# Kernel tuning notes

Measured on AMD Instinct MI355X. Metric: run time of the kernel, lower is better.

## Reference

```python
import jax, jax.numpy as jnp
import numpy as np


def setup_inputs() -> dict:
    key = jax.random.key(0)
    kx, kw = jax.random.split(key)
    B, IN, OUT = 8192, 256, 16384
    x = jax.random.normal(kx, (B, IN), dtype=jnp.float32)
    weight = jax.random.normal(kw, (OUT, IN), dtype=jnp.float32)
    return {"x": x, "weight": weight}


def reference(x, weight):
    # Pairwise Euclidean distance ||x_b - w_o||_2 via expansion:
    temperature = 2.0
    x2 = jnp.sum(x * x, axis=1, keepdims=True)          # [B, 1]
    w2 = jnp.sum(weight * weight, axis=1)[None, :]       # [1, OUT]
    xw = x @ weight.T                                    # [B, OUT]
    d2 = jnp.maximum(x2 + w2 - 2.0 * xw, 0.0)            # clamp fp error
    dist = jnp.sqrt(d2)                                  # [B, OUT]
    return jax.nn.softmax(-temperature * dist, axis=1)
```

## Files before the change

kernel.cpp:

```cpp
#include <hip/hip_runtime.h>
#include <math.h>
#include <stdint.h>

#define M_ROWS 8192
#define N_COLS 16384
#define K_DIM  256
#define NTILE  (N_COLS / 128)
#define CHUNK  2048
#define NCHUNK 4

typedef _Float16 half8  __attribute__((ext_vector_type(8)));
typedef _Float16 half4v __attribute__((ext_vector_type(4)));
typedef float    vf4    __attribute__((ext_vector_type(4)));

__device__ __forceinline__ void gload16(const void* g, void* lds) {
  __builtin_amdgcn_global_load_lds(
      (__attribute__((address_space(1))) void*)(void*)g,
      (__attribute__((address_space(3))) void*)lds, 16, 0, 0);
}

__global__ __launch_bounds__(256) void prep_kernel(
    const float* __restrict__ x, const float* __restrict__ w,
    float* __restrict__ x2, float* __restrict__ w2,
    _Float16* __restrict__ xh, _Float16* __restrict__ wh) {
  int row  = blockIdx.x * 4 + (threadIdx.x >> 6);
  int lane = threadIdx.x & 63;
  const float* src; _Float16* dst; float* nrm;
  if (row < M_ROWS) {
    src = x + (size_t)row * K_DIM; dst = xh + (size_t)row * K_DIM; nrm = x2 + row;
  } else {
    int r = row - M_ROWS;
    src = w + (size_t)r * K_DIM; dst = wh + (size_t)r * K_DIM; nrm = w2 + r;
  }
  float4 v = ((const float4*)src)[lane];
  float s = v.x*v.x + v.y*v.y + v.z*v.z + v.w*v.w;
  #pragma unroll
  for (int off = 32; off > 0; off >>= 1) s += __shfl_down(s, off);
  if (lane == 0) *nrm = s;
  half4v h; h[0]=(_Float16)v.x; h[1]=(_Float16)v.y; h[2]=(_Float16)v.z; h[3]=(_Float16)v.w;
  ((half4v*)dst)[lane] = h;
}

template <int MODE>
__global__ __launch_bounds__(256, 2) void gemm_pass(
    const _Float16* __restrict__ A, const _Float16* __restrict__ Bm,
    const float* __restrict__ x2g, const float* __restrict__ w2g,
    const float* __restrict__ invg,
    float* __restrict__ partials,
    float* __restrict__ out) {
  __shared__ _Float16 As[128 * 64];
  __shared__ _Float16 Bs[128 * 64];
  __shared__ float x2s[128];
  __shared__ float w2s[128];
  __shared__ float invs[128];
  __shared__ float rowpart[2][128];

  int id   = blockIdx.x;
  int xcd  = id & 7;
  int rest = id >> 3;
  int ct   = xcd * 16 + (rest & 15);
  int rt   = rest >> 4;
  int brow = rt * 128;
  int bcol = ct * 128;

  int tid = threadIdx.x, lane = tid & 63, wid = tid >> 6;
  int wr = wid >> 1, wc = wid & 1;

  if (tid < 128) {
    x2s[tid] = x2g[brow + tid];
    if (MODE == 1) invs[tid] = invg[brow + tid];
  } else {
    w2s[tid - 128] = w2g[bcol + tid - 128];
  }

  vf4 acc[4][4] = {};

  for (int kk = 0; kk < K_DIM; kk += 64) {
    #pragma unroll
    for (int i = 0; i < 4; ++i) {
      int seg = wid * 4 + i;
      int r   = seg * 8 + (lane >> 3);
      gload16(A  + (size_t)(brow + r) * K_DIM + kk + (lane & 7) * 8, (char*)As + seg * 1024);
      gload16(Bm + (size_t)(bcol + r) * K_DIM + kk + (lane & 7) * 8, (char*)Bs + seg * 1024);
    }
    __syncthreads();

    #pragma unroll
    for (int ks = 0; ks < 2; ++ks) {
      half8 af[4], bf[4];
      #pragma unroll
      for (int m = 0; m < 4; ++m)
        af[m] = *(const half8*)&As[(wr*64 + m*16 + (lane & 15)) * 64 + ks*32 + (lane >> 4) * 8];
      #pragma unroll
      for (int n = 0; n < 4; ++n)
        bf[n] = *(const half8*)&Bs[(wc*64 + n*16 + (lane & 15)) * 64 + ks*32 + (lane >> 4) * 8];
      #pragma unroll
      for (int m = 0; m < 4; ++m)
        #pragma unroll
        for (int n = 0; n < 4; ++n)
          acc[m][n] = __builtin_amdgcn_mfma_f32_16x16x32_f16(af[m], bf[n], acc[m][n], 0, 0, 0);
    }
    __syncthreads();
  }

  if (MODE == 0) {
    #pragma unroll
    for (int m = 0; m < 4; ++m) {
      #pragma unroll
      for (int j = 0; j < 4; ++j) {
        int rl = wr * 64 + m * 16 + ((lane >> 4) << 2) + j;
        float x2v = x2s[rl];
        float sm = 0.f;
        #pragma unroll
        for (int n = 0; n < 4; ++n) {
          int cl = wc * 64 + n * 16 + (lane & 15);
          float d2 = fmaxf(x2v + w2s[cl] - 2.0f * acc[m][n][j], 0.0f);
          sm += __expf(-2.0f * sqrtf(d2));
        }
        sm += __shfl_xor(sm, 1);
        sm += __shfl_xor(sm, 2);
        sm += __shfl_xor(sm, 4);
        sm += __shfl_xor(sm, 8);
        if ((lane & 15) == 0) rowpart[wc][rl] = sm;
      }
    }
    __syncthreads();
    if (tid < 128)
      partials[(size_t)(brow + tid) * NTILE + ct] = rowpart[0][tid] + rowpart[1][tid];
  } else {
    #pragma unroll
    for (int m = 0; m < 4; ++m) {
      #pragma unroll
      for (int j = 0; j < 4; ++j) {
        int rl = wr * 64 + m * 16 + ((lane >> 4) << 2) + j;
        float x2v = x2s[rl];
        float inv = invs[rl];
        size_t rowbase = (size_t)(brow + rl) * N_COLS + bcol;
        #pragma unroll
        for (int n = 0; n < 4; ++n) {
          int cl = wc * 64 + n * 16 + (lane & 15);
          float d2 = fmaxf(x2v + w2s[cl] - 2.0f * acc[m][n][j], 0.0f);
          out[rowbase + cl] = __expf(-2.0f * sqrtf(d2)) * inv;
        }
      }
    }
  }
}

__global__ __launch_bounds__(256) void reduce_inv(
    const float* __restrict__ partials, float* __restrict__ invg) {
  int row  = blockIdx.x * 4 + (threadIdx.x >> 6);
  int lane = threadIdx.x & 63;
  const float* p = partials + (size_t)row * NTILE;
  float s = p[lane] + p[lane + 64];
  #pragma unroll
  for (int off = 32; off > 0; off >>= 1) s += __shfl_down(s, off);
  if (lane == 0) invg[row] = 1.0f / s;
}

template <bool WS>
__global__ __launch_bounds__(256, 2) void gemm_logit(
    const void* __restrict__ Aptr, const void* __restrict__ Bptr,
    const float* __restrict__ x2g, const float* __restrict__ w2g,
    float* __restrict__ out, int mbase) {
  __shared__ _Float16 As[128 * 64];
  __shared__ _Float16 Bs[128 * 64];
  __shared__ float x2s[128];
  __shared__ float w2s[128];

  int id  = blockIdx.x;
  int xcd = id & 7;
  int rt  = (id >> 3) & 15;
  int c2  = id >> 7;
  int brow = mbase + rt * 128;
  int bcol = (xcd * 16 + c2) * 128;

  int tid = threadIdx.x, lane = tid & 63, wid = tid >> 6;
  int wr = wid >> 1, wc = wid & 1;

  vf4 acc[4][4] = {};

  const float* xf = (const float*)Aptr;
  const float* wf = (const float*)Bptr;
  {
    const float* src = (tid < 128) ? xf + (size_t)(brow + tid) * K_DIM
                                   : wf + (size_t)(bcol + tid - 128) * K_DIM;
    float s = 0.f;
    for (int i = 0; i < 64; ++i) {
      float4 v = ((const float4*)src)[i];
      s += v.x*v.x + v.y*v.y + v.z*v.z + v.w*v.w;
    }
    if (tid < 128) x2s[tid] = s; else w2s[tid - 128] = s;
  }

  for (int kk = 0; kk < K_DIM; kk += 64) {
    #pragma unroll
    for (int i = 0; i < 8; ++i) {
      int idx = i * 256 + tid;
      int r = idx >> 4, kq = idx & 15;
      float4 va = ((const float4*)(xf + (size_t)(brow + r) * K_DIM + kk))[kq];
      float4 vb = ((const float4*)(wf + (size_t)(bcol + r) * K_DIM + kk))[kq];
      half4v ha; ha[0]=(_Float16)va.x; ha[1]=(_Float16)va.y; ha[2]=(_Float16)va.z; ha[3]=(_Float16)va.w;
      half4v hb; hb[0]=(_Float16)vb.x; hb[1]=(_Float16)vb.y; hb[2]=(_Float16)vb.z; hb[3]=(_Float16)vb.w;
      *(half4v*)&As[r * 64 + kq * 4] = ha;
      *(half4v*)&Bs[r * 64 + kq * 4] = hb;
    }
    __syncthreads();
    #pragma unroll
    for (int ks = 0; ks < 2; ++ks) {
      half8 af[4], bf[4];
      #pragma unroll
      for (int m = 0; m < 4; ++m)
        af[m] = *(const half8*)&As[(wr*64 + m*16 + (lane & 15)) * 64 + ks*32 + (lane >> 4) * 8];
      #pragma unroll
      for (int n = 0; n < 4; ++n)
        bf[n] = *(const half8*)&Bs[(wc*64 + n*16 + (lane & 15)) * 64 + ks*32 + (lane >> 4) * 8];
      #pragma unroll
      for (int m = 0; m < 4; ++m)
        #pragma unroll
        for (int n = 0; n < 4; ++n)
          acc[m][n] = __builtin_amdgcn_mfma_f32_16x16x32_f16(af[m], bf[n], acc[m][n], 0, 0, 0);
    }
    __syncthreads();
  }

  #pragma unroll
  for (int m = 0; m < 4; ++m) {
    int rl = wr * 64 + m * 16 + ((lane >> 4) << 2);
    #pragma unroll
    for (int n = 0; n < 4; ++n) {
      int cl = wc * 64 + n * 16 + (lane & 15);
      int c  = bcol + cl;
      float w2v = w2s[cl];
      #pragma unroll
      for (int j = 0; j < 4; ++j) {
        int r = brow + rl + j;
        float x2v = x2s[rl + j];
        float d2 = fmaxf(x2v + w2v - 2.0f * acc[m][n][j], 0.0f);
        out[(size_t)r * N_COLS + c] = -2.0f * sqrtf(d2);
      }
    }
  }
}

__global__ __launch_bounds__(256) void softmax_norm(float* __restrict__ io, int mbase) {
  int row = mbase + blockIdx.x;
  float* p = io + (size_t)row * N_COLS;
  int tid = threadIdx.x;
  __shared__ float wsum[4];

  float4 v[16];
  float s = 0.f;
  #pragma unroll
  for (int i = 0; i < 16; ++i) {
    v[i] = ((const float4*)p)[i * 256 + tid];
    v[i].x = __expf(v[i].x); v[i].y = __expf(v[i].y);
    v[i].z = __expf(v[i].z); v[i].w = __expf(v[i].w);
    s += v[i].x + v[i].y + v[i].z + v[i].w;
  }
  #pragma unroll
  for (int off = 32; off > 0; off >>= 1) s += __shfl_down(s, off);
  if ((tid & 63) == 0) wsum[tid >> 6] = s;
  __syncthreads();
  float inv = 1.0f / (wsum[0] + wsum[1] + wsum[2] + wsum[3]);
  #pragma unroll
  for (int i = 0; i < 16; ++i) {
    float4 o = v[i];
    o.x *= inv; o.y *= inv; o.z *= inv; o.w *= inv;
    ((float4*)p)[i * 256 + tid] = o;
  }
}

extern "C" void kernel_launch(void* const* d_in, const int* in_sizes, int n_in,
                              void* d_out, int out_size, void* d_ws, size_t ws_size,
                              hipStream_t stream) {
  const float* x = (const float*)d_in[0];
  const float* w = (const float*)d_in[1];
  float* out = (float*)d_out;

  char* ws = (char*)d_ws;
  float* x2 = (float*)ws;
  float* w2 = x2 + M_ROWS;
  float* invsum = w2 + N_COLS;
  float* partials = invsum + M_ROWS;
  _Float16* xh = (_Float16*)(partials + (size_t)M_ROWS * NTILE);
  _Float16* wh = xh + (size_t)M_ROWS * K_DIM;
  const size_t need = ((size_t)(M_ROWS + N_COLS + M_ROWS) + (size_t)M_ROWS * NTILE) * 4
                    + (size_t)(M_ROWS + N_COLS) * K_DIM * 2;
  const bool useWS = (ws_size >= need);

  if (useWS) {
    prep_kernel<<<(M_ROWS + N_COLS) / 4, 256, 0, stream>>>(x, w, x2, w2, xh, wh);
    gemm_pass<0><<<(M_ROWS / 128) * (N_COLS / 128), 256, 0, stream>>>(
        xh, wh, x2, w2, nullptr, partials, nullptr);
    reduce_inv<<<M_ROWS / 4, 256, 0, stream>>>(partials, invsum);
    gemm_pass<1><<<(M_ROWS / 128) * (N_COLS / 128), 256, 0, stream>>>(
        xh, wh, x2, w2, invsum, nullptr, out);
  } else {
    for (int c = 0; c < NCHUNK; ++c) {
      int mbase = c * CHUNK;
      gemm_logit<false><<<(CHUNK / 128) * (N_COLS / 128), 256, 0, stream>>>(
          x, w, nullptr, nullptr, out, mbase);
      softmax_norm<<<CHUNK, 256, 0, stream>>>(out, mbase);
    }
  }
}
```

Measured before the change: 333.8 us.

## Store fp16 dot products in first pass and finalize softmax elementwise

When the workspace is large enough, the first GEMM pass also writes the raw x·w products as fp16 to a full B×OUT buffer. A new grid-stride finalize kernel then reads that buffer to compute exp(-2·dist)·inv and write the output, replacing the second GEMM recompute pass. This removes the repeated matrix multiply but adds a large intermediate write and read, and it rounds the dot products to fp16 before the distance is formed. The fallback paths are kept, with the chunked kernel renamed and simplified.

```diff
diff --git a/kernel.cpp b/kernel.cpp
--- a/kernel.cpp
+++ b/kernel.cpp
@@ -47,6 +47,7 @@
     const float* __restrict__ x2g, const float* __restrict__ w2g,
     const float* __restrict__ invg,
     float* __restrict__ partials,
+    _Float16* __restrict__ xwout,
     float* __restrict__ out) {
   __shared__ _Float16 As[128 * 64];
   __shared__ _Float16 Bs[128 * 64];
@@ -103,19 +104,22 @@
     __syncthreads();
   }
 
-  if (MODE == 0) {
+  if (MODE == 0 || MODE == 2) {
     #pragma unroll
     for (int m = 0; m < 4; ++m) {
       #pragma unroll
       for (int j = 0; j < 4; ++j) {
         int rl = wr * 64 + m * 16 + ((lane >> 4) << 2) + j;
         float x2v = x2s[rl];
+        size_t rowbase = (size_t)(brow + rl) * N_COLS + bcol;
         float sm = 0.f;
         #pragma unroll
         for (int n = 0; n < 4; ++n) {
           int cl = wc * 64 + n * 16 + (lane & 15);
-          float d2 = fmaxf(x2v + w2s[cl] - 2.0f * acc[m][n][j], 0.0f);
+          float xwv = acc[m][n][j];
+          float d2 = fmaxf(x2v + w2s[cl] - 2.0f * xwv, 0.0f);
           sm += __expf(-2.0f * sqrtf(d2));
+          if (MODE == 2) xwout[rowbase + cl] = (_Float16)xwv;
         }
         sm += __shfl_xor(sm, 1);
         sm += __shfl_xor(sm, 2);
@@ -158,10 +162,37 @@
   if (lane == 0) invg[row] = 1.0f / s;
 }
 
-template <bool WS>
-__global__ __launch_bounds__(256, 2) void gemm_logit(
-    const void* __restrict__ Aptr, const void* __restrict__ Bptr,
-    const float* __restrict__ x2g, const float* __restrict__ w2g,
+__global__ __launch_bounds__(256) void finalize_kernel(
+    const _Float16* __restrict__ xw, const float* __restrict__ x2g,
+    const float* __restrict__ w2g, const float* __restrict__ invg,
+    float* __restrict__ out) {
+  const size_t NV = (size_t)M_ROWS * N_COLS / 8;
+  size_t stride = (size_t)gridDim.x * blockDim.x;
+  for (size_t i = (size_t)blockIdx.x * blockDim.x + threadIdx.x; i < NV; i += stride) {
+    size_t base = i * 8;
+    int row = (int)(base >> 14);
+    int col = (int)(base & (N_COLS - 1));
+    half8 h = *(const half8*)(xw + base);
+    float x2v = x2g[row];
+    float inv = invg[row];
+    float4 wa = *(const float4*)(w2g + col);
+    float4 wb = *(const float4*)(w2g + col + 4);
+    float4 o0, o1;
+    o0.x = __expf(-2.f * sqrtf(fmaxf(x2v + wa.x - 2.f * (float)h[0], 0.f))) * inv;
+    o0.y = __expf(-2.f * sqrtf(fmaxf(x2v + wa.y - 2.f * (float)h[1], 0.f))) * inv;
+    o0.z = __expf(-2.f * sqrtf(fmaxf(x2v + wa.z - 2.f * (float)h[2], 0.f))) * inv;
+    o0.w = __expf(-2.f * sqrtf(fmaxf(x2v + wa.w - 2.f * (float)h[3], 0.f))) * inv;
+    o1.x = __expf(-2.f * sqrtf(fmaxf(x2v + wb.x - 2.f * (float)h[4], 0.f))) * inv;
+    o1.y = __expf(-2.f * sqrtf(fmaxf(x2v + wb.y - 2.f * (float)h[5], 0.f))) * inv;
+    o1.z = __expf(-2.f * sqrtf(fmaxf(x2v + wb.z - 2.f * (float)h[6], 0.f))) * inv;
+    o1.w = __expf(-2.f * sqrtf(fmaxf(x2v + wb.w - 2.f * (float)h[7], 0.f))) * inv;
+    *(float4*)(out + base)     = o0;
+    *(float4*)(out + base + 4) = o1;
+  }
+}
+
+__global__ __launch_bounds__(256, 2) void gemm_logit_f32(
+    const float* __restrict__ xf, const float* __restrict__ wf,
     float* __restrict__ out, int mbase) {
   __shared__ _Float16 As[128 * 64];
   __shared__ _Float16 Bs[128 * 64];
@@ -180,8 +211,6 @@
 
   vf4 acc[4][4] = {};
 
-  const float* xf = (const float*)Aptr;
-  const float* wf = (const float*)Bptr;
   {
     const float* src = (tid < 128) ? xf + (size_t)(brow + tid) * K_DIM
                                    : wf + (size_t)(bcol + tid - 128) * K_DIM;
@@ -235,8 +264,7 @@
       #pragma unroll
       for (int j = 0; j < 4; ++j) {
         int r = brow + rl + j;
-        float x2v = x2s[rl + j];
-        float d2 = fmaxf(x2v + w2v - 2.0f * acc[m][n][j], 0.0f);
+        float d2 = fmaxf(x2s[rl + j] + w2v - 2.0f * acc[m][n][j], 0.0f);
         out[(size_t)r * N_COLS + c] = -2.0f * sqrtf(d2);
       }
     }
@@ -285,22 +313,29 @@
   float* partials = invsum + M_ROWS;
   _Float16* xh = (_Float16*)(partials + (size_t)M_ROWS * NTILE);
   _Float16* wh = xh + (size_t)M_ROWS * K_DIM;
-  const size_t need = ((size_t)(M_ROWS + N_COLS + M_ROWS) + (size_t)M_ROWS * NTILE) * 4
-                    + (size_t)(M_ROWS + N_COLS) * K_DIM * 2;
-  const bool useWS = (ws_size >= need);
-
-  if (useWS) {
+  _Float16* xw = wh + (size_t)N_COLS * K_DIM;
+  const size_t needB = ((size_t)(M_ROWS + N_COLS + M_ROWS) + (size_t)M_ROWS * NTILE) * 4
+                     + (size_t)(M_ROWS + N_COLS) * K_DIM * 2;
+  const size_t needA = needB + (size_t)M_ROWS * N_COLS * 2;
+
+  if (ws_size >= needA) {
+    prep_kernel<<<(M_ROWS + N_COLS) / 4, 256, 0, stream>>>(x, w, x2, w2, xh, wh);
+    gemm_pass<2><<<(M_ROWS / 128) * (N_COLS / 128), 256, 0, stream>>>(
+        xh, wh, x2, w2, nullptr, partials, xw, nullptr);
+    reduce_inv<<<M_ROWS / 4, 256, 0, stream>>>(partials, invsum);
+    finalize_kernel<<<2048, 256, 0, stream>>>(xw, x2, w2, invsum, out);
+  } else if (ws_size >= needB) {
     prep_kernel<<<(M_ROWS + N_COLS) / 4, 256, 0, stream>>>(x, w, x2, w2, xh, wh);
     gemm_pass<0><<<(M_ROWS / 128) * (N_COLS / 128), 256, 0, stream>>>(
-        xh, wh, x2, w2, nullptr, partials, nullptr);
+        xh, wh, x2, w2, nullptr, partials, nullptr, nullptr);
     reduce_inv<<<M_ROWS / 4, 256, 0, stream>>>(partials, invsum);
     gemm_pass<1><<<(M_ROWS / 128) * (N_COLS / 128), 256, 0, stream>>>(
-        xh, wh, x2, w2, invsum, nullptr, out);
+        xh, wh, x2, w2, invsum, nullptr, nullptr, out);
   } else {
     for (int c = 0; c < NCHUNK; ++c) {
       int mbase = c * CHUNK;
-      gemm_logit<false><<<(CHUNK / 128) * (N_COLS / 128), 256, 0, stream>>>(
-          x, w, nullptr, nullptr, out, mbase);
+      gemm_logit_f32<<<(CHUNK / 128) * (N_COLS / 128), 256, 0, stream>>>(
+          x, w, out, mbase);
       softmax_norm<<<CHUNK, 256, 0, stream>>>(out, mbase);
     }
   }
```

After: 400.2 us. 19.9% more time.

## Enlarge GEMM tiles to 256x256x128 with swizzled LDS layout

Applied to the files above, without the earlier changes.

The two gemm_pass kernels move from 128x128 tiles with BK=64 and 256 threads to 256x256 tiles with BK=128 and 512 threads. Each wave now holds 8x4 accumulators. LDS rows are XOR-swizzled on both the global-to-LDS load and the fragment reads to avoid bank conflicts. The partial-sum reduction is adapted to 64 column tiles. The larger tiles raise data reuse and cut global traffic, but they use 128KB of LDS per block and more registers, which may limit occupancy and latency hiding.

```diff
diff --git a/kernel.cpp b/kernel.cpp
--- a/kernel.cpp
+++ b/kernel.cpp
@@ -5,7 +5,10 @@
 #define M_ROWS 8192
 #define N_COLS 16384
 #define K_DIM  256
-#define NTILE  (N_COLS / 128)
+#define BM     256
+#define BN     256
+#define BK     128
+#define NTILE  (N_COLS / BN)
 #define CHUNK  2048
 #define NCHUNK 4
 
@@ -17,6 +20,10 @@
   __builtin_amdgcn_global_load_lds(
       (__attribute__((address_space(1))) void*)(void*)g,
       (__attribute__((address_space(3))) void*)lds, 16, 0, 0);
+}
+
+__device__ __forceinline__ int swz_addr(int row, int colbyte) {
+  return (row << 8) + (colbyte ^ ((row & 7) << 4));
 }
 
 __global__ __launch_bounds__(256) void prep_kernel(
@@ -42,60 +49,62 @@
 }
 
 template <int MODE>
-__global__ __launch_bounds__(256, 2) void gemm_pass(
+__global__ __launch_bounds__(512, 2) void gemm_pass(
     const _Float16* __restrict__ A, const _Float16* __restrict__ Bm,
     const float* __restrict__ x2g, const float* __restrict__ w2g,
     const float* __restrict__ invg,
     float* __restrict__ partials,
     float* __restrict__ out) {
-  __shared__ _Float16 As[128 * 64];
-  __shared__ _Float16 Bs[128 * 64];
-  __shared__ float x2s[128];
-  __shared__ float w2s[128];
-  __shared__ float invs[128];
-  __shared__ float rowpart[2][128];
+  __shared__ _Float16 As[BM * BK];
+  __shared__ _Float16 Bs[BN * BK];
+  __shared__ float x2s[BM];
+  __shared__ float w2s[BN];
+  __shared__ float invs[BM];
+  __shared__ float rowpart[4][BM];
 
   int id   = blockIdx.x;
   int xcd  = id & 7;
   int rest = id >> 3;
-  int ct   = xcd * 16 + (rest & 15);
-  int rt   = rest >> 4;
-  int brow = rt * 128;
-  int bcol = ct * 128;
+  int ct   = xcd * 8 + (rest & 7);
+  int rt   = rest >> 3;
+  int brow = rt * BM;
+  int bcol = ct * BN;
 
   int tid = threadIdx.x, lane = tid & 63, wid = tid >> 6;
-  int wr = wid >> 1, wc = wid & 1;
-
-  if (tid < 128) {
+  int wr = wid >> 2, wc = wid & 3;
+
+  if (tid < BM) {
     x2s[tid] = x2g[brow + tid];
     if (MODE == 1) invs[tid] = invg[brow + tid];
   } else {
-    w2s[tid - 128] = w2g[bcol + tid - 128];
-  }
-
-  vf4 acc[4][4] = {};
-
-  for (int kk = 0; kk < K_DIM; kk += 64) {
-    #pragma unroll
-    for (int i = 0; i < 4; ++i) {
-      int seg = wid * 4 + i;
-      int r   = seg * 8 + (lane >> 3);
-      gload16(A  + (size_t)(brow + r) * K_DIM + kk + (lane & 7) * 8, (char*)As + seg * 1024);
-      gload16(Bm + (size_t)(bcol + r) * K_DIM + kk + (lane & 7) * 8, (char*)Bs + seg * 1024);
-    }
-    __syncthreads();
-
-    #pragma unroll
-    for (int ks = 0; ks < 2; ++ks) {
-      half8 af[4], bf[4];
-      #pragma unroll
-      for (int m = 0; m < 4; ++m)
-        af[m] = *(const half8*)&As[(wr*64 + m*16 + (lane & 15)) * 64 + ks*32 + (lane >> 4) * 8];
+    w2s[tid - BM] = w2g[bcol + tid - BM];
+  }
+
+  vf4 acc[8][4] = {};
+
+  for (int kk = 0; kk < K_DIM; kk += BK) {
+    #pragma unroll
+    for (int i = 0; i < 8; ++i) {
+      int seg = i * 8 + wid;
+      int row = seg * 4 + (lane >> 4);
+      int colhalf = ((lane & 15) * 8) ^ ((row & 7) << 3);
+      gload16(A  + (size_t)(brow + row) * K_DIM + kk + colhalf, (char*)As + seg * 1024);
+      gload16(Bm + (size_t)(bcol + row) * K_DIM + kk + colhalf, (char*)Bs + seg * 1024);
+    }
+    __syncthreads();
+
+    #pragma unroll
+    for (int ks = 0; ks < 4; ++ks) {
+      int colbyte = ks * 64 + (lane >> 4) * 16;
+      half8 af[8], bf[4];
+      #pragma unroll
+      for (int m = 0; m < 8; ++m)
+        af[m] = *(const half8*)((const char*)As + swz_addr(wr * 128 + m * 16 + (lane & 15), colbyte));
       #pragma unroll
       for (int n = 0; n < 4; ++n)
-        bf[n] = *(const half8*)&Bs[(wc*64 + n*16 + (lane & 15)) * 64 + ks*32 + (lane >> 4) * 8];
-      #pragma unroll
-      for (int m = 0; m < 4; ++m)
+        bf[n] = *(const half8*)((const char*)Bs + swz_addr(wc * 64 + n * 16 + (lane & 15), colbyte));
+      #pragma unroll
+      for (int m = 0; m < 8; ++m)
         #pragma unroll
         for (int n = 0; n < 4; ++n)
           acc[m][n] = __builtin_amdgcn_mfma_f32_16x16x32_f16(af[m], bf[n], acc[m][n], 0, 0, 0);
@@ -105,10 +114,10 @@
 
   if (MODE == 0) {
     #pragma unroll
-    for (int m = 0; m < 4; ++m) {
+    for (int m = 0; m < 8; ++m) {
       #pragma unroll
       for (int j = 0; j < 4; ++j) {
-        int rl = wr * 64 + m * 16 + ((lane >> 4) << 2) + j;
+        int rl = wr * 128 + m * 16 + ((lane >> 4) << 2) + j;
         float x2v = x2s[rl];
         float sm = 0.f;
         #pragma unroll
@@ -125,14 +134,15 @@
       }
     }
     __syncthreads();
-    if (tid < 128)
-      partials[(size_t)(brow + tid) * NTILE + ct] = rowpart[0][tid] + rowpart[1][tid];
+    if (tid < BM)
+      partials[(size_t)(brow + tid) * NTILE + ct] =
+          rowpart[0][tid] + rowpart[1][tid] + rowpart[2][tid] + rowpart[3][tid];
   } else {
     #pragma unroll
-    for (int m = 0; m < 4; ++m) {
+    for (int m = 0; m < 8; ++m) {
       #pragma unroll
       for (int j = 0; j < 4; ++j) {
-        int rl = wr * 64 + m * 16 + ((lane >> 4) << 2) + j;
+        int rl = wr * 128 + m * 16 + ((lane >> 4) << 2) + j;
         float x2v = x2s[rl];
         float inv = invs[rl];
         size_t rowbase = (size_t)(brow + rl) * N_COLS + bcol;
@@ -152,16 +162,14 @@
   int row  = blockIdx.x * 4 + (threadIdx.x >> 6);
   int lane = threadIdx.x & 63;
   const float* p = partials + (size_t)row * NTILE;
-  float s = p[lane] + p[lane + 64];
+  float s = p[lane];
   #pragma unroll
   for (int off = 32; off > 0; off >>= 1) s += __shfl_down(s, off);
   if (lane == 0) invg[row] = 1.0f / s;
 }
 
-template <bool WS>
-__global__ __launch_bounds__(256, 2) void gemm_logit(
-    const void* __restrict__ Aptr, const void* __restrict__ Bptr,
-    const float* __restrict__ x2g, const float* __restrict__ w2g,
+__global__ __launch_bounds__(256, 2) void gemm_logit_f32(
+    const float* __restrict__ xf, const float* __restrict__ wf,
     float* __restrict__ out, int mbase) {
   __shared__ _Float16 As[128 * 64];
   __shared__ _Float16 Bs[128 * 64];
@@ -180,8 +188,6 @@
 
   vf4 acc[4][4] = {};
 
-  const float* xf = (const float*)Aptr;
-  const float* wf = (const float*)Bptr;
   {
     const float* src = (tid < 128) ? xf + (size_t)(brow + tid) * K_DIM
                                    : wf + (size_t)(bcol + tid - 128) * K_DIM;
@@ -235,8 +241,7 @@
       #pragma unroll
       for (int j = 0; j < 4; ++j) {
         int r = brow + rl + j;
-        float x2v = x2s[rl + j];
-        float d2 = fmaxf(x2v + w2v - 2.0f * acc[m][n][j], 0.0f);
+        float d2 = fmaxf(x2s[rl + j] + w2v - 2.0f * acc[m][n][j], 0.0f);
         out[(size_t)r * N_COLS + c] = -2.0f * sqrtf(d2);
       }
     }
@@ -287,20 +292,19 @@
   _Float16* wh = xh + (size_t)M_ROWS * K_DIM;
   const size_t need = ((size_t)(M_ROWS + N_COLS + M_ROWS) + (size_t)M_ROWS * NTILE) * 4
                     + (size_t)(M_ROWS + N_COLS) * K_DIM * 2;
-  const bool useWS = (ws_size >= need);
-
-  if (useWS) {
+
+  if (ws_size >= need) {
     prep_kernel<<<(M_ROWS + N_COLS) / 4, 256, 0, stream>>>(x, w, x2, w2, xh, wh);
-    gemm_pass<0><<<(M_ROWS / 128) * (N_COLS / 128), 256, 0, stream>>>(
+    gemm_pass<0><<<(M_ROWS / BM) * (N_COLS / BN), 512, 0, stream>>>(
         xh, wh, x2, w2, nullptr, partials, nullptr);
     reduce_inv<<<M_ROWS / 4, 256, 0, stream>>>(partials, invsum);
-    gemm_pass<1><<<(M_ROWS / 128) * (N_COLS / 128), 256, 0, stream>>>(
+    gemm_pass<1><<<(M_ROWS / BM) * (N_COLS / BN), 512, 0, stream>>>(
         xh, wh, x2, w2, invsum, nullptr, out);
   } else {
     for (int c = 0; c < NCHUNK; ++c) {
       int mbase = c * CHUNK;
-      gemm_logit<false><<<(CHUNK / 128) * (N_COLS / 128), 256, 0, stream>>>(
-          x, w, nullptr, nullptr, out, mbase);
+      gemm_logit_f32<<<(CHUNK / 128) * (N_COLS / 128), 256, 0, stream>>>(
+          x, w, out, mbase);
       softmax_norm<<<CHUNK, 256, 0, stream>>>(out, mbase);
     }
   }
```

After: 392.3 us. 1.18x slower.
